# Optimization experiments

Measured on AMD Instinct MI355X. Metric: run time of the kernel, lower is better.

## Reference

```python
import jax, jax.numpy as jnp
import numpy as np


def setup_inputs() -> dict:
    key = jax.random.key(0)
    k1, k2, k3 = jax.random.split(key, 3)
    B, C, H, W = 16, 256, 128, 128
    r = 16  # channels // reduction
    x = jax.random.normal(k1, (B, C, H, W), dtype=jnp.float32)
    # 1x1 conv kernels flattened to linear weights (fan-in scaled init)
    w1 = jax.random.normal(k2, (r, C), dtype=jnp.float32) * (1.0 / np.sqrt(C))
    b1 = jnp.zeros((r,), dtype=jnp.float32)
    w2 = jax.random.normal(k3, (C, r), dtype=jnp.float32) * (1.0 / np.sqrt(r))
    b2 = jnp.zeros((C,), dtype=jnp.float32)
    return {"x": x, "w1": w1, "b1": b1, "w2": w2, "b2": b2}


def reference(x, w1, b1, w2, b2):
    b, c, h, w = x.shape
    n = h * w
    x_flat = x.reshape(b, c, n)
    mu = x_flat.mean(axis=2, keepdims=True)
    xc = x_flat - mu  # [b, c, n]
    # v[b,i] = mean_j cov[b,i,j] where cov = xc @ xc^T / (n-1).
    # Algebraic reassociation: mean_j sum_k xc[i,k] xc[j,k] = sum_k xc[i,k] * s[k] / c
    # with s[k] = sum_j xc[j,k]. Avoids the O(C^2 * n) bmm; same math.
    s = xc.sum(axis=1)  # [b, n]
    denom = jnp.float32(max(1, n - 1) * c)
    v = jnp.einsum('bcn,bn->bc', xc, s) / denom  # [b, c]
    # MLP of 1x1 convs on a [b,c,1,1] descriptor == two linear layers
    h1 = jax.nn.relu(v @ w1.T + b1)              # [b, r]
    gate = jax.nn.sigmoid(h1 @ w2.T + b2)        # [b, c]
    return x * gate[:, :, None, None]
```

## Files before the change

kernel.cpp:

```cpp
#include <hip/hip_runtime.h>

#define B_ 16
#define C_ 256
#define N_ 16384
#define R_ 16
#define SUB_ 32

typedef float f32x4 __attribute__((ext_vector_type(4)));

__device__ __forceinline__ float4 ldf4(const float* p) {
    return *reinterpret_cast<const float4*>(p);
}

template<int NSUB>
__global__ __launch_bounds__(256)
void kA(const float* __restrict__ x,
        float* __restrict__ Ppart,
        float* __restrict__ RSpart,
        int blocksPerBatch) {
    const int blk = blockIdx.x;
    const int b = blockIdx.y;
    const int t = threadIdx.x;
    const int kq = t & 7;
    const int crow = t >> 3;

    __shared__ float tile[C_][33];
    __shared__ float csp[8][32];
    __shared__ float colsum[SUB_];

    const float* xb = x + (size_t)b * C_ * N_
                    + (size_t)blk * (NSUB * SUB_) + (kq << 2);

    float4 pA[8], pB[8];
    float accP = 0.f, accRS = 0.f;

#pragma unroll
    for (int r = 0; r < 8; ++r)
        pA[r] = ldf4(xb + (size_t)(crow + (r << 5)) * N_);

#define PHASE(CUR, NXT, S)                                                     \
    {                                                                          \
               \
        if ((S) + 1 < NSUB) {                                                  \
            _Pragma("unroll")                                                  \
            for (int r = 0; r < 8; ++r)                                        \
                NXT[r] = ldf4(xb + (size_t)(crow + (r << 5)) * N_              \
                              + ((S) + 1) * SUB_);                             \
        }                                                                      \
        _Pragma("unroll")                                                      \
        for (int r = 0; r < 8; ++r)                                            \
            *reinterpret_cast<float4*>(&tile[crow + (r << 5)][kq << 2]) = CUR[r]; \
        asm volatile("s_waitcnt lgkmcnt(0)" ::: "memory");                     \
        __builtin_amdgcn_s_barrier();                                          \
        {     \
            const int n = t & 31, oct = t >> 5;                                \
            float cs = 0.f;                                                    \
            _Pragma("unroll")                                                  \
            for (int i = 0; i < 32; ++i) cs += tile[(oct << 5) + i][n];        \
            csp[oct][n] = cs;                                                  \
        }                                                                      \
        asm volatile("s_waitcnt lgkmcnt(0)" ::: "memory");                     \
        __builtin_amdgcn_s_barrier();                                          \
        if (t < SUB_) {                                                        \
            float cs = 0.f;                                                    \
            _Pragma("unroll")                                                  \
            for (int o = 0; o < 8; ++o) cs += csp[o][t];                       \
            colsum[t] = cs;                                                    \
        }                                                                      \
        asm volatile("s_waitcnt lgkmcnt(0)" ::: "memory");                     \
        __builtin_amdgcn_s_barrier();                                          \
        _Pragma("unroll")                                                      \
        for (int j = 0; j < 8; ++j) {           \
            float4 xv = *reinterpret_cast<float4*>(&tile[t][j << 2]);          \
            float4 cl = *reinterpret_cast<float4*>(&colsum[j << 2]);           \
            accP += xv.x * cl.x + xv.y * cl.y + xv.z * cl.z + xv.w * cl.w;     \
            accRS += xv.x + xv.y + xv.z + xv.w;                                \
        }                                                                      \
        __builtin_amdgcn_s_barrier();   \
    }

    for (int s = 0; s < NSUB; s += 2) {
        PHASE(pA, pB, s)
        PHASE(pB, pA, s + 1)
    }
#undef PHASE

    const size_t base = ((size_t)b * blocksPerBatch + blk) * C_;
    Ppart [base + t] = accP;
    RSpart[base + t] = accRS;
}

__global__ void kB(const float* __restrict__ Ppart,
                   const float* __restrict__ RSpart,
                   const float* __restrict__ w1, const float* __restrict__ b1,
                   const float* __restrict__ w2, const float* __restrict__ b2,
                   float* __restrict__ gate, int blocksPerBatch) {
    const int b = blockIdx.x;
    const int t = threadIdx.x;

    float P = 0.f, RS = 0.f;
    for (int k = 0; k < blocksPerBatch; ++k) {
        P  += Ppart [((size_t)b * blocksPerBatch + k) * C_ + t];
        RS += RSpart[((size_t)b * blocksPerBatch + k) * C_ + t];
    }

    __shared__ float red[4];
    float s = RS;
#pragma unroll
    for (int off = 32; off; off >>= 1) s += __shfl_down(s, off, 64);
    if ((t & 63) == 0) red[t >> 6] = s;
    __syncthreads();
    const float T = red[0] + red[1] + red[2] + red[3];
    const float M = T / (float)N_;
    const float denom = (float)(N_ - 1) * (float)C_;

    __shared__ float vl[C_];
    vl[t] = (P - M * RS) / denom;
    __syncthreads();

    __shared__ float hpart[R_][16];
    __shared__ float h1[R_];
    {
        const int i = t >> 4, cc = t & 15;
        float a = 0.f;
#pragma unroll
        for (int k = 0; k < 16; ++k)
            a += vl[(cc << 4) + k] * w1[i * C_ + (cc << 4) + k];
        hpart[i][cc] = a;
    }
    __syncthreads();
    if (t < R_) {
        float a = b1[t];
#pragma unroll
        for (int k = 0; k < 16; ++k) a += hpart[t][k];
        h1[t] = a > 0.f ? a : 0.f;
    }
    __syncthreads();

    float a = b2[t];
#pragma unroll
    for (int i = 0; i < R_; ++i) a += h1[i] * w2[t * R_ + i];
    gate[b * C_ + t] = 1.f / (1.f + __expf(-a));
}

__global__ void kC(const float* __restrict__ x,
                   const float* __restrict__ gate,
                   float* __restrict__ out) {
    const size_t total4 = (size_t)B_ * C_ * N_ / 4;
    for (size_t i = (size_t)blockIdx.x * blockDim.x + threadIdx.x; i < total4;
         i += (size_t)gridDim.x * blockDim.x) {
        const int bc = (int)(i >> 12);
        const float g = gate[bc];
        float4 vx = reinterpret_cast<const float4*>(x)[i];
        f32x4 r;
        r.x = vx.x * g; r.y = vx.y * g; r.z = vx.z * g; r.w = vx.w * g;
        __builtin_nontemporal_store(r, reinterpret_cast<f32x4*>(out) + i);
    }
}

extern "C" void kernel_launch(void* const* d_in, const int* in_sizes, int n_in,
                              void* d_out, int out_size, void* d_ws, size_t ws_size,
                              hipStream_t stream) {
    (void)in_sizes; (void)n_in; (void)out_size; (void)ws_size;
    const float* x  = (const float*)d_in[0];
    const float* w1 = (const float*)d_in[1];
    const float* b1 = (const float*)d_in[2];
    const float* w2 = (const float*)d_in[3];
    const float* b2 = (const float*)d_in[4];
    float* out = (float*)d_out;

    const int bpb = 64;

    float* ws     = (float*)d_ws;
    float* Ppart  = ws;
    float* RSpart = Ppart + (size_t)B_ * bpb * C_;
    float* gate   = RSpart + (size_t)B_ * bpb * C_;

    hipLaunchKernelGGL((kA<8>), dim3(bpb, B_), dim3(256), 0, stream,
                       x, Ppart, RSpart, bpb);
    hipLaunchKernelGGL(kB, dim3(B_), dim3(256), 0, stream,
                       Ppart, RSpart, w1, b1, w2, b2, gate, bpb);
    hipLaunchKernelGGL(kC, dim3(2048), dim3(256), 0, stream,
                       x, gate, out);
}
```

Baseline: 157.8 us.

## Compute column sums in registers with wave shuffles instead of LDS tile transpose

The stats kernel no longer stages each 256x32 sub-tile through shared memory. Column sums are now formed from register-held float4 loads via cross-lane xor shuffles, then combined across the four waves through a tiny shared buffer. The per-channel dot products accumulate per register row and are shuffle-reduced at the end. This removes most LDS traffic and two of the three barriers per phase, at the cost of more shuffle instructions and extra accumulator registers.

```diff
diff --git a/kernel.cpp b/kernel.cpp
--- a/kernel.cpp
+++ b/kernel.cpp
@@ -23,16 +23,18 @@
     const int t = threadIdx.x;
     const int kq = t & 7;
     const int crow = t >> 3;
-
-    __shared__ float tile[C_][33];
-    __shared__ float csp[8][32];
-    __shared__ float colsum[SUB_];
+    const int lane = t & 63;
+    const int wave = t >> 6;
+
+    __shared__ float cw[4][8][4];
 
     const float* xb = x + (size_t)b * C_ * N_
                     + (size_t)blk * (NSUB * SUB_) + (kq << 2);
 
     float4 pA[8], pB[8];
-    float accP = 0.f, accRS = 0.f;
+    float accP[8], accRS[8];
+#pragma unroll
+    for (int r = 0; r < 8; ++r) { accP[r] = 0.f; accRS[r] = 0.f; }
 
 #pragma unroll
     for (int r = 0; r < 8; ++r)
@@ -40,43 +42,47 @@
 
 #define PHASE(CUR, NXT, S)                                                     \
     {                                                                          \
-               \
         if ((S) + 1 < NSUB) {                                                  \
             _Pragma("unroll")                                                  \
             for (int r = 0; r < 8; ++r)                                        \
                 NXT[r] = ldf4(xb + (size_t)(crow + (r << 5)) * N_              \
                               + ((S) + 1) * SUB_);                             \
         }                                                                      \
+               \
+        float4 cs = CUR[0];                                                    \
         _Pragma("unroll")                                                      \
-        for (int r = 0; r < 8; ++r)                                            \
-            *reinterpret_cast<float4*>(&tile[crow + (r << 5)][kq << 2]) = CUR[r]; \
+        for (int r = 1; r < 8; ++r) {                                          \
+            cs.x += CUR[r].x; cs.y += CUR[r].y;                                \
+            cs.z += CUR[r].z; cs.w += CUR[r].w;                                \
+        }                                                                      \
+        _Pragma("unroll")                                                      \
+        for (int m = 8; m <= 32; m <<= 1) {                                    \
+            cs.x += __shfl_xor(cs.x, m, 64);                                   \
+            cs.y += __shfl_xor(cs.y, m, 64);                                   \
+            cs.z += __shfl_xor(cs.z, m, 64);                                   \
+            cs.w += __shfl_xor(cs.w, m, 64);                                   \
+        }                                                                      \
+        if (lane < 8)                                                          \
+            *reinterpret_cast<float4*>(&cw[wave][lane][0]) =                   \
+                make_float4(cs.x, cs.y, cs.z, cs.w);                           \
         asm volatile("s_waitcnt lgkmcnt(0)" ::: "memory");                     \
         __builtin_amdgcn_s_barrier();                                          \
-        {     \
-            const int n = t & 31, oct = t >> 5;                                \
-            float cs = 0.f;                                                    \
-            _Pragma("unroll")                                                  \
-            for (int i = 0; i < 32; ++i) cs += tile[(oct << 5) + i][n];        \
-            csp[oct][n] = cs;                                                  \
+        float4 c0 = *reinterpret_cast<const float4*>(&cw[0][kq][0]);           \
+        float4 c1 = *reinterpret_cast<const float4*>(&cw[1][kq][0]);           \
+        float4 c2 = *reinterpret_cast<const float4*>(&cw[2][kq][0]);           \
+        float4 c3 = *reinterpret_cast<const float4*>(&cw[3][kq][0]);           \
+        float4 cl = make_float4(c0.x + c1.x + c2.x + c3.x,                     \
+                                c0.y + c1.y + c2.y + c3.y,                     \
+                                c0.z + c1.z + c2.z + c3.z,                     \
+                                c0.w + c1.w + c2.w + c3.w);                    \
+        _Pragma("unroll")                                                      \
+        for (int r = 0; r < 8; ++r) {                                          \
+            accP[r] += CUR[r].x * cl.x + CUR[r].y * cl.y                       \
+                     + CUR[r].z * cl.z + CUR[r].w * cl.w;                      \
+            accRS[r] += CUR[r].x + CUR[r].y + CUR[r].z + CUR[r].w;             \
         }                                                                      \
         asm volatile("s_waitcnt lgkmcnt(0)" ::: "memory");                     \
-        __builtin_amdgcn_s_barrier();                                          \
-        if (t < SUB_) {                                                        \
-            float cs = 0.f;                                                    \
-            _Pragma("unroll")                                                  \
-            for (int o = 0; o < 8; ++o) cs += csp[o][t];                       \
-            colsum[t] = cs;                                                    \
-        }                                                                      \
-        asm volatile("s_waitcnt lgkmcnt(0)" ::: "memory");                     \
-        __builtin_amdgcn_s_barrier();                                          \
-        _Pragma("unroll")                                                      \
-        for (int j = 0; j < 8; ++j) {           \
-            float4 xv = *reinterpret_cast<float4*>(&tile[t][j << 2]);          \
-            float4 cl = *reinterpret_cast<float4*>(&colsum[j << 2]);           \
-            accP += xv.x * cl.x + xv.y * cl.y + xv.z * cl.z + xv.w * cl.w;     \
-            accRS += xv.x + xv.y + xv.z + xv.w;                                \
-        }                                                                      \
-        __builtin_amdgcn_s_barrier();   \
+        __builtin_amdgcn_s_barrier();     \
     }
 
     for (int s = 0; s < NSUB; s += 2) {
@@ -85,9 +91,22 @@
     }
 #undef PHASE
 
-    const size_t base = ((size_t)b * blocksPerBatch + blk) * C_;
-    Ppart [base + t] = accP;
-    RSpart[base + t] = accRS;
+#pragma unroll
+    for (int r = 0; r < 8; ++r) {
+#pragma unroll
+        for (int m = 1; m <= 4; m <<= 1) {
+            accP[r]  += __shfl_xor(accP[r],  m, 64);
+            accRS[r] += __shfl_xor(accRS[r], m, 64);
+        }
+    }
+    if (kq == 0) {
+        const size_t base = ((size_t)b * blocksPerBatch + blk) * C_;
+#pragma unroll
+        for (int r = 0; r < 8; ++r) {
+            Ppart [base + crow + (r << 5)] = accP[r];
+            RSpart[base + crow + (r << 5)] = accRS[r];
+        }
+    }
 }
 
 __global__ void kB(const float* __restrict__ Ppart,
```

Result: no change. 155.4 us (-1.5%).
